# Performance work log

Measured on AMD Instinct MI355X. Metric: run time of the kernel, lower is better.

The kernel has to match this reference:

```python
import jax, jax.numpy as jnp
import numpy as np

N, H, C, E, R = 16384, 1024, 256, 16, 128
EPS = 1e-8


def setup_inputs() -> dict:
    key = jax.random.key(0)
    ks = jax.random.split(key, 8)
    s = 1.0 / np.sqrt(H)
    return {
        "x": jax.random.normal(ks[0], (N, H), jnp.float32),
        "Wd": jax.random.normal(ks[1], (H, C), jnp.float32) * s,
        "bd": jax.random.normal(ks[2], (C,), jnp.float32) * 0.01,
        "centroids": jax.random.uniform(ks[3], (E, C), jnp.float32),  # torch.rand
        "Wg": jax.random.normal(ks[4], (E, H, H), jnp.float32) * s,
        "bg": jax.random.normal(ks[5], (E, H), jnp.float32) * 0.01,
        "U": jax.random.normal(ks[6], (E, H, R), jnp.float32) * s,
        "V": jax.random.normal(ks[7], (E, R, H), jnp.float32) * (1.0 / np.sqrt(R)),
        "k": 2,
    }


def reference(x, Wd, bd, centroids, Wg, bg, U, V, k):
    # ---- Router ----
    distilled = jax.nn.gelu(x @ Wd + bd, approximate=False)          # [N, C]
    dn = distilled / jnp.maximum(
        jnp.linalg.norm(distilled, axis=-1, keepdims=True), EPS)
    cn = centroids / jnp.maximum(
        jnp.linalg.norm(centroids, axis=-1, keepdims=True), EPS)
    # cdist (euclidean) between dn [N,C] and cn [E,C]
    d2 = (jnp.sum(dn * dn, -1, keepdims=True)
          + jnp.sum(cn * cn, -1)[None, :]
          - 2.0 * (dn @ cn.T))                                        # [N, E]
    distances = jnp.sqrt(jnp.maximum(d2, 0.0))
    probabilities = jax.nn.softmax(-distances, axis=-1)               # [N, E]
    top_p, top_i = jax.lax.top_k(probabilities, k)                    # [N, k]
    # sparse combine weights: zero except at top-k experts
    combine = jnp.zeros((x.shape[0], E), x.dtype)
    combine = combine.at[jnp.arange(x.shape[0])[:, None], top_i].set(top_p)
    # ---- Expert dispatch: scan over experts (low-rank Highway blocks) ----
    def body(acc, params):
        Wg_e, bg_e, U_e, V_e, w_e = params
        gate = jax.nn.sigmoid(x @ Wg_e + bg_e)                        # [N, H]
        trans = (x @ U_e) @ V_e                                       # [N, H]
        y = gate * trans + (1.0 - gate) * x
        return acc + w_e[:, None] * y, None
    out, _ = jax.lax.scan(body, jnp.zeros_like(x),
                          (Wg, bg, U, V, combine.T))
    return out
```

## Files before the change

### kernel.cpp

```cpp
#include <hip/hip_runtime.h>
#include <hip/hip_bf16.h>
#include <cstdint>
#include <cstddef>

#define NTOK 16384
#define HD   1024
#define CD   256
#define NE   16
#define RD   128

typedef __attribute__((ext_vector_type(8))) short bf16x8;
typedef __attribute__((ext_vector_type(4))) float f32x4;
typedef unsigned short u16;
typedef unsigned int u32;

__device__ __forceinline__ u16 f2bf(float f) {
    u32 u = __float_as_uint(f);
    u32 r = (u + 0x7FFFu + ((u >> 16) & 1u)) >> 16;
    return (u16)r;
}

__device__ __forceinline__ void gload16(const void* g, void* lds) {
    __builtin_amdgcn_global_load_lds((const __attribute__((address_space(1))) void*)g,
                                     (__attribute__((address_space(3))) void*)lds,
                                     16, 0, 0);
}

__device__ __forceinline__ float wredsum(float v) {
#pragma unroll
    for (int m = 32; m >= 1; m >>= 1) v += __shfl_xor(v, m, 64);
    return v;
}

__global__ __launch_bounds__(64) void centroid_norm_kernel(
    const float* __restrict__ cen, float* __restrict__ cn, float* __restrict__ sncn)
{
    int e = blockIdx.x, l = threadIdx.x;
    float4 c = *(const float4*)&cen[e * CD + l * 4];
    float ss = wredsum(c.x * c.x + c.y * c.y + c.z * c.z + c.w * c.w);
    float den = fmaxf(sqrtf(ss), 1e-8f);
    float4 n;
    n.x = c.x / den; n.y = c.y / den; n.z = c.z / den; n.w = c.w / den;
    *(float4*)&cn[e * CD + l * 4] = n;
    float s2 = wredsum(n.x * n.x + n.y * n.y + n.z * n.z + n.w * n.w);
    if (l == 0) sncn[e] = s2;
}

__global__ __launch_bounds__(256, 4) void router_gemm_kernel(
    const float* __restrict__ x, const float* __restrict__ Wd,
    const float* __restrict__ bd, float* __restrict__ dT)
{
    __shared__ float lA[16][128];
    __shared__ float lB[16][64];
    int tid = threadIdx.x;
    int rb = (blockIdx.x >> 2) * 128;
    int cb = (blockIdx.x & 3) * 64;
    int tx = tid & 15, ty = tid >> 4;
    int arow = tid >> 1, akq = (tid & 1) * 8;
    int bk = tid >> 4, bc = (tid & 15) * 4;
    float acc[8][4];
#pragma unroll
    for (int i = 0; i < 8; ++i)
#pragma unroll
        for (int j = 0; j < 4; ++j) acc[i][j] = 0.f;

    for (int k0 = 0; k0 < HD; k0 += 16) {
        float4 a0 = *(const float4*)&x[(size_t)(rb + arow) * HD + k0 + akq];
        float4 a1 = *(const float4*)&x[(size_t)(rb + arow) * HD + k0 + akq + 4];
        float4 bv = *(const float4*)&Wd[(size_t)(k0 + bk) * CD + cb + bc];
        __syncthreads();
        lA[akq + 0][arow] = a0.x; lA[akq + 1][arow] = a0.y;
        lA[akq + 2][arow] = a0.z; lA[akq + 3][arow] = a0.w;
        lA[akq + 4][arow] = a1.x; lA[akq + 5][arow] = a1.y;
        lA[akq + 6][arow] = a1.z; lA[akq + 7][arow] = a1.w;
        *(float4*)&lB[bk][bc] = bv;
        __syncthreads();
#pragma unroll
        for (int kk = 0; kk < 16; ++kk) {
            float4 va0 = *(const float4*)&lA[kk][ty * 8];
            float4 va1 = *(const float4*)&lA[kk][ty * 8 + 4];
            float4 vb  = *(const float4*)&lB[kk][tx * 4];
            float ar[8] = {va0.x, va0.y, va0.z, va0.w, va1.x, va1.y, va1.z, va1.w};
            float br[4] = {vb.x, vb.y, vb.z, vb.w};
#pragma unroll
            for (int i = 0; i < 8; ++i)
#pragma unroll
                for (int j = 0; j < 4; ++j) acc[i][j] = fmaf(ar[i], br[j], acc[i][j]);
        }
    }
#pragma unroll
    for (int j = 0; j < 4; ++j) {
        int c = cb + tx * 4 + j;
        float b = bd[c];
        float g[8];
#pragma unroll
        for (int i = 0; i < 8; ++i) {
            float v = acc[i][j] + b;
            g[i] = 0.5f * v * (1.f + erff(v * 0.70710678118654752f));
        }
        float4 w0 = {g[0], g[1], g[2], g[3]};
        float4 w1 = {g[4], g[5], g[6], g[7]};
        *(float4*)&dT[(size_t)c * NTOK + rb + ty * 8] = w0;
        *(float4*)&dT[(size_t)c * NTOK + rb + ty * 8 + 4] = w1;
    }
}

__global__ __launch_bounds__(256) void router_score_kernel(
    const float* __restrict__ dT, const float* __restrict__ cn,
    const float* __restrict__ sncn, int* __restrict__ top_i,
    float* __restrict__ top_w, int* __restrict__ counts)
{
    __shared__ float lcn[NE][CD];
    __shared__ float sdot[NE][64];
    __shared__ float sss[64];
    __shared__ int hist[NE];
    int tid = threadIdx.x, lane = tid & 63, w = tid >> 6;
    for (int i = tid; i < NE * CD / 4; i += 256)
        ((float4*)&lcn[0][0])[i] = ((const float4*)cn)[i];
    if (tid < NE) hist[tid] = 0;
    __syncthreads();

    int tokbase = blockIdx.x * 64;
    const float* p = dT + tokbase + lane;
    int e0 = w * 4;
    float d0 = 0.f, d1 = 0.f, d2a = 0.f, d3 = 0.f, ss = 0.f;
#pragma unroll 4
    for (int k = 0; k < CD; ++k) {
        float v = p[(size_t)k * NTOK];
        ss = fmaf(v, v, ss);
        d0 = fmaf(v, lcn[e0 + 0][k], d0);
        d1 = fmaf(v, lcn[e0 + 1][k], d1);
        d2a = fmaf(v, lcn[e0 + 2][k], d2a);
        d3 = fmaf(v, lcn[e0 + 3][k], d3);
    }
    sdot[e0 + 0][lane] = d0;
    sdot[e0 + 1][lane] = d1;
    sdot[e0 + 2][lane] = d2a;
    sdot[e0 + 3][lane] = d3;
    if (w == 0) sss[lane] = ss;
    __syncthreads();

    if (tid < 64) {
        int tok = tokbase + tid;
        float ssv = sss[tid];
        float den = fmaxf(sqrtf(ssv), 1e-8f);
        float inv = 1.f / den;
        float sndn = (ssv * inv) * inv;
        float pr[NE];
#pragma unroll
        for (int e = 0; e < NE; ++e) {
            float dotn = sdot[e][tid] * inv;
            float dd2 = sndn + sncn[e] - 2.f * dotn;
            pr[e] = -sqrtf(fmaxf(dd2, 0.f));
        }
        float mx = pr[0];
#pragma unroll
        for (int e = 1; e < NE; ++e) mx = fmaxf(mx, pr[e]);
        float sum = 0.f;
#pragma unroll
        for (int e = 0; e < NE; ++e) { pr[e] = expf(pr[e] - mx); sum += pr[e]; }
        float invs = 1.f / sum;
#pragma unroll
        for (int e = 0; e < NE; ++e) pr[e] *= invs;
        int i1 = 0; float p1 = pr[0];
#pragma unroll
        for (int e = 1; e < NE; ++e) if (pr[e] > p1) { p1 = pr[e]; i1 = e; }
        int i2 = -1; float p2 = -1.f;
#pragma unroll
        for (int e = 0; e < NE; ++e) if (e != i1 && pr[e] > p2) { p2 = pr[e]; i2 = e; }
        top_i[tok * 2 + 0] = i1; top_w[tok * 2 + 0] = p1;
        top_i[tok * 2 + 1] = i2; top_w[tok * 2 + 1] = p2;
        atomicAdd(&hist[i1], 1);
        atomicAdd(&hist[i2], 1);
    }
    __syncthreads();
    if (tid < NE) atomicAdd(&counts[tid], hist[tid]);
}

__global__ void scan_kernel(const int* __restrict__ counts, int* __restrict__ offsets,
                            int* __restrict__ blkstart, int* __restrict__ cursor)
{
    if (threadIdx.x == 0 && blockIdx.x == 0) {
        int o = 0, b = 0;
        for (int e = 0; e < NE; ++e) {
            offsets[e] = o; blkstart[e] = b; cursor[e] = 0;
            o += counts[e]; b += (counts[e] + 63) >> 6;
        }
        offsets[NE] = o; blkstart[NE] = b;
    }
}

__global__ __launch_bounds__(256) void build_lists_kernel(
    const int* __restrict__ top_i, const float* __restrict__ top_w,
    const int* __restrict__ offsets, int* __restrict__ cursor,
    int* __restrict__ list_tok, float* __restrict__ list_w)
{
    int t = blockIdx.x * 256 + threadIdx.x;
#pragma unroll
    for (int j = 0; j < 2; ++j) {
        int e = top_i[t * 2 + j];
        int pos = atomicAdd(&cursor[e], 1);
        int idx = offsets[e] + pos;
        list_tok[idx] = t;
        list_w[idx] = top_w[t * 2 + j];
    }
}

__global__ __launch_bounds__(256) void cvt_bf16_kernel(
    const float* __restrict__ src, u16* __restrict__ dst, int n4)
{
    int i = blockIdx.x * 256 + threadIdx.x;
    if (i >= n4) return;
    float4 v = *(const float4*)&src[(size_t)i * 4];
    ushort4 o;
    o.x = f2bf(v.x); o.y = f2bf(v.y); o.z = f2bf(v.z); o.w = f2bf(v.w);
    *(ushort4*)&dst[(size_t)i * 4] = o;
}

__global__ __launch_bounds__(256) void transpose_cvt_kernel(
    const float* __restrict__ src, u16* __restrict__ dst, int K, int N)
{
    __shared__ float t[32][33];
    const float* s = src + (size_t)blockIdx.z * K * N;
    u16* d = dst + (size_t)blockIdx.z * K * N;
    int kb = blockIdx.y * 32, nb = blockIdx.x * 32;
    int r = threadIdx.x >> 3, c4 = (threadIdx.x & 7) * 4;
    float4 v = *(const float4*)&s[(size_t)(kb + r) * N + nb + c4];
    t[r][c4 + 0] = v.x; t[r][c4 + 1] = v.y; t[r][c4 + 2] = v.z; t[r][c4 + 3] = v.w;
    __syncthreads();
    ushort4 o;
    o.x = f2bf(t[c4 + 0][r]); o.y = f2bf(t[c4 + 1][r]);
    o.z = f2bf(t[c4 + 2][r]); o.w = f2bf(t[c4 + 3][r]);
    *(ushort4*)&d[(size_t)(nb + r) * K + kb + c4] = o;
}


__global__ __launch_bounds__(256, 3) void tproj_kernel(
    const u16* __restrict__ xbf, const u16* __restrict__ uT,
    const int* __restrict__ list_tok, const int* __restrict__ offsets,
    const int* __restrict__ blkstart, u16* __restrict__ tbf)
{
    __shared__ __align__(16) u16 lds[2 * 6144];
    __shared__ int s_tok[64];
    int mb = blockIdx.x;
    int e = 0;
#pragma unroll
    for (int i = 0; i < NE; ++i) if (mb >= blkstart[i + 1]) e = i + 1;
    if (e >= NE) return;
    int mloc = (mb - blkstart[e]) * 64;
    int base = offsets[e] + mloc;
    int cnt = offsets[e + 1] - offsets[e];
    int mv = min(64, cnt - mloc);
    int tid = threadIdx.x, lane = tid & 63, w = tid >> 6;
    if (tid < 64) s_tok[tid] = list_tok[base + (tid < mv ? tid : 0)];
    __syncthreads();
    int lrow = lane >> 2;
    int sl = (lane & 3) ^ ((lane >> 3) & 3);
    int rr = lane & 15, hi = lane >> 4;
    int rslot = hi ^ ((rr >> 1) & 3);
    const u16* uE = uT + (size_t)e * RD * HD;

    const u16* gb[3]; char* lp[3];
#pragma unroll
    for (int i = 0; i < 3; ++i) {
        int idx = w + 4 * i;
        if (idx < 4) {
            gb[i] = xbf + (size_t)s_tok[idx * 16 + lrow] * HD + sl * 8;
            lp[i] = (char*)lds + idx * 1024;
        } else {
            int bi = idx - 4;
            gb[i] = uE + (size_t)(bi * 16 + lrow) * HD + sl * 8;
            lp[i] = (char*)lds + 4096 + bi * 1024;
        }
    }
    const f32x4 zz = {0.f, 0.f, 0.f, 0.f};
    f32x4 acc[4][2];
#pragma unroll
    for (int im = 0; im < 4; ++im)
#pragma unroll
        for (int in = 0; in < 2; ++in) acc[im][in] = zz;

    auto STAGE = [&](int buf, int t) {
#pragma unroll
        for (int i = 0; i < 3; ++i) gload16(gb[i] + t * 32, lp[i] + buf * 12288);
    };
    auto COMP = [&](int buf, f32x4 (&a)[4][2]) {
        const u16* LA = lds + buf * 6144;
        const u16* LB = LA + 2048;
        bf16x8 af[4], bfv[2];
#pragma unroll
        for (int im = 0; im < 4; ++im) af[im] = *(const bf16x8*)&LA[(im * 16 + rr) * 32 + rslot * 8];
#pragma unroll
        for (int in = 0; in < 2; ++in) bfv[in] = *(const bf16x8*)&LB[(w * 32 + in * 16 + rr) * 32 + rslot * 8];
#pragma unroll
        for (int im = 0; im < 4; ++im)
#pragma unroll
            for (int in = 0; in < 2; ++in)
                a[im][in] = __builtin_amdgcn_mfma_f32_16x16x32_bf16(af[im], bfv[in], a[im][in], 0, 0, 0);
    };

    STAGE(0, 0);
    __syncthreads();
    for (int t = 0; t < 31; ++t) {
        STAGE((t + 1) & 1, t + 1);
        COMP(t & 1, acc);
        __syncthreads();
    }
    COMP(1, acc);

#pragma unroll
    for (int im = 0; im < 4; ++im)
#pragma unroll
        for (int in = 0; in < 2; ++in)
#pragma unroll
            for (int j = 0; j < 4; ++j) {
                int r = im * 16 + hi * 4 + j;
                if (r < mv) {
                    int c = w * 32 + in * 16 + rr;
                    tbf[(size_t)(base + r) * RD + c] = f2bf(acc[im][in][j]);
                }
            }
}

__global__ __launch_bounds__(256, 3) void expert_kernel(
    const u16* __restrict__ xbf, const u16* __restrict__ wgT,
    const u16* __restrict__ vT, const u16* __restrict__ tbf,
    const float* __restrict__ x, const float* __restrict__ bg,
    const int* __restrict__ list_tok, const float* __restrict__ list_w,
    const int* __restrict__ offsets, const int* __restrict__ blkstart,
    float* __restrict__ out)
{
    __shared__ __align__(16) u16 lds[2 * 6144];
    __shared__ int s_tok[64];
    __shared__ float s_w[64];
    int mb = blockIdx.x >> 3, ct = blockIdx.x & 7;
    int e = 0;
#pragma unroll
    for (int i = 0; i < NE; ++i) if (mb >= blkstart[i + 1]) e = i + 1;
    if (e >= NE) return;
    int mloc = (mb - blkstart[e]) * 64;
    int base = offsets[e] + mloc;
    int cnt = offsets[e + 1] - offsets[e];
    int mv = min(64, cnt - mloc);
    int tid = threadIdx.x, lane = tid & 63, w = tid >> 6;
    if (tid < 64) {
        int p = base + (tid < mv ? tid : 0);
        s_tok[tid] = list_tok[p];
        s_w[tid] = (tid < mv) ? list_w[p] : 0.f;
    }
    __syncthreads();
    int lrow = lane >> 2;
    int sl = (lane & 3) ^ ((lane >> 3) & 3);
    int rr = lane & 15, hi = lane >> 4;
    int rslot = hi ^ ((rr >> 1) & 3);

    const u16* wgE = wgT + (size_t)e * HD * HD + (size_t)(ct * 128) * HD;
    const u16* vE  = vT  + (size_t)e * HD * RD + (size_t)(ct * 128) * RD;

    char* lp[3];
    const u16* gbT[3]; const u16* gbG[3];
#pragma unroll
    for (int i = 0; i < 3; ++i) {
        int idx = w + 4 * i;
        if (idx < 4) {
            lp[i]  = (char*)lds + idx * 1024;
            gbT[i] = tbf + (size_t)(base + idx * 16 + lrow) * RD + sl * 8;
            gbG[i] = xbf + (size_t)s_tok[idx * 16 + lrow] * HD + sl * 8;
        } else {
            int bi = idx - 4;
            lp[i]  = (char*)lds + 4096 + bi * 1024;
            gbT[i] = vE  + (size_t)(bi * 16 + lrow) * RD + sl * 8;
            gbG[i] = wgE + (size_t)(bi * 16 + lrow) * HD + sl * 8;
        }
    }

    auto STAGE = [&](int buf, int t, const u16* const (&gb)[3]) {
#pragma unroll
        for (int i = 0; i < 3; ++i) gload16(gb[i] + t * 32, lp[i] + buf * 12288);
    };
    auto COMP = [&](int buf, f32x4 (&a)[4][2]) {
        const u16* LA = lds + buf * 6144;
        const u16* LB = LA + 2048;
        bf16x8 af[4], bfv[2];
#pragma unroll
        for (int im = 0; im < 4; ++im) af[im] = *(const bf16x8*)&LA[(im * 16 + rr) * 32 + rslot * 8];
#pragma unroll
        for (int in = 0; in < 2; ++in) bfv[in] = *(const bf16x8*)&LB[(w * 32 + in * 16 + rr) * 32 + rslot * 8];
#pragma unroll
        for (int im = 0; im < 4; ++im)
#pragma unroll
            for (int in = 0; in < 2; ++in)
                a[im][in] = __builtin_amdgcn_mfma_f32_16x16x32_bf16(af[im], bfv[in], a[im][in], 0, 0, 0);
    };

    const f32x4 zz = {0.f, 0.f, 0.f, 0.f};
    f32x4 accT[4][2];
#pragma unroll
    for (int im = 0; im < 4; ++im)
#pragma unroll
        for (int in = 0; in < 2; ++in) accT[im][in] = zz;

    STAGE(0, 0, gbT);
    __syncthreads();
#pragma unroll
    for (int t = 0; t < 3; ++t) {
        STAGE((t + 1) & 1, t + 1, gbT);
        COMP(t & 1, accT);
        __syncthreads();
    }
    STAGE(0, 0, gbG);
    COMP(1, accT);
    __syncthreads();

    f32x4 accG[4][2];
#pragma unroll
    for (int im = 0; im < 4; ++im)
#pragma unroll
        for (int in = 0; in < 2; ++in) accG[im][in] = zz;

    for (int t = 0; t < 31; ++t) {
        STAGE((t + 1) & 1, t + 1, gbG);
        COMP(t & 1, accG);
        __syncthreads();
    }
    COMP(1, accG);

    float bgv[2];
#pragma unroll
    for (int in = 0; in < 2; ++in)
        bgv[in] = bg[e * HD + ct * 128 + w * 32 + in * 16 + rr];

#pragma unroll
    for (int im = 0; im < 4; ++im)
#pragma unroll
        for (int j = 0; j < 4; ++j) {
            int r = im * 16 + hi * 4 + j;
            if (r < mv) {
                int tok = s_tok[r];
                float wgt = s_w[r];
                size_t rowoff = (size_t)tok * HD;
#pragma unroll
                for (int in = 0; in < 2; ++in) {
                    int c = ct * 128 + w * 32 + in * 16 + rr;
                    float gp = accG[im][in][j] + bgv[in];
                    float sg = 1.f / (1.f + __expf(-gp));
                    float tr = accT[im][in][j];
                    float xv = x[rowoff + c];
                    float yv = sg * tr + (1.f - sg) * xv;
                    atomicAdd(&out[rowoff + c], wgt * yv);
                }
            }
        }
}

extern "C" void kernel_launch(void* const* d_in, const int* in_sizes, int n_in,
                              void* d_out, int out_size, void* d_ws, size_t ws_size,
                              hipStream_t stream)
{
    const float* x   = (const float*)d_in[0];
    const float* Wd  = (const float*)d_in[1];
    const float* bd  = (const float*)d_in[2];
    const float* cen = (const float*)d_in[3];
    const float* Wg  = (const float*)d_in[4];
    const float* bg  = (const float*)d_in[5];
    const float* U   = (const float*)d_in[6];
    const float* V   = (const float*)d_in[7];
    float* out = (float*)d_out;

    char* ws = (char*)d_ws;
    size_t off = 0;
    auto alloc = [&](size_t bytes) { size_t o = off; off = (off + bytes + 255) & ~(size_t)255; return o; };
    float* dT        = (float*)(ws + alloc((size_t)NTOK * CD * 4));
    float* cn        = (float*)(ws + alloc((size_t)NE * CD * 4));
    float* sncn      = (float*)(ws + alloc(NE * 4));
    int*   top_i     = (int*)(ws + alloc((size_t)NTOK * 2 * 4));
    float* top_w     = (float*)(ws + alloc((size_t)NTOK * 2 * 4));
    int*   counts    = (int*)(ws + alloc(NE * 4));
    int*   offsets   = (int*)(ws + alloc((NE + 1) * 4));
    int*   blkstart  = (int*)(ws + alloc((NE + 1) * 4));
    int*   cursor    = (int*)(ws + alloc(NE * 4));
    int*   list_tok  = (int*)(ws + alloc((size_t)NTOK * 2 * 4));
    float* list_w    = (float*)(ws + alloc((size_t)NTOK * 2 * 4));
    u16*   xbf       = (u16*)(ws + alloc((size_t)NTOK * HD * 2));
    u16*   wgT       = (u16*)(ws + alloc((size_t)NE * HD * HD * 2));
    u16*   uT        = (u16*)(ws + alloc((size_t)NE * RD * HD * 2));
    u16*   vT        = (u16*)(ws + alloc((size_t)NE * RD * HD * 2));
    u16*   tbf       = (u16*)(ws + alloc(((size_t)NTOK * 2 + 64) * RD * 2));

    hipMemsetAsync(out, 0, (size_t)out_size * 4, stream);
    hipMemsetAsync(counts, 0, NE * 4, stream);

    centroid_norm_kernel<<<NE, 64, 0, stream>>>(cen, cn, sncn);
    router_gemm_kernel<<<(NTOK / 128) * 4, 256, 0, stream>>>(x, Wd, bd, dT);
    router_score_kernel<<<NTOK / 64, 256, 0, stream>>>(dT, cn, sncn, top_i, top_w, counts);
    scan_kernel<<<1, 64, 0, stream>>>(counts, offsets, blkstart, cursor);
    build_lists_kernel<<<NTOK / 256, 256, 0, stream>>>(top_i, top_w, offsets, cursor, list_tok, list_w);

    cvt_bf16_kernel<<<(NTOK * HD / 4 + 255) / 256, 256, 0, stream>>>(x, xbf, NTOK * HD / 4);
    transpose_cvt_kernel<<<dim3(HD / 32, HD / 32, NE), 256, 0, stream>>>(Wg, wgT, HD, HD);
    transpose_cvt_kernel<<<dim3(RD / 32, HD / 32, NE), 256, 0, stream>>>(U, uT, HD, RD);
    transpose_cvt_kernel<<<dim3(HD / 32, RD / 32, NE), 256, 0, stream>>>(V, vT, RD, HD);

    int maxblk = NTOK * 2 / 64 + NE;
    tproj_kernel<<<maxblk, 256, 0, stream>>>(xbf, uT, list_tok, offsets, blkstart, tbf);
    expert_kernel<<<maxblk * 8, 256, 0, stream>>>(xbf, wgT, vT, tbf, x, bg,
                                                  list_tok, list_w, offsets, blkstart, out);
}
```

Measured before the change: 579.1 us.

## Widen expert tile to 256 columns, remap blocks for XCD locality, reorder gate/trans GEMMs

The expert kernel's per-block output width doubles from 128 to 256 columns (4x4 MFMA accumulators per wave), so each staged token tile is reused across twice as many weight columns and x-row gathers are halved. Block indices are remapped so blocks sharing a column tile are grouped, presumably for L2/XCD locality. The gate GEMM now runs first, with its sigmoid results packed to fp16 to free registers before the trans accumulation. The costs are higher register pressure, more LDS per block, lower occupancy, and fp16 rounding of the gate values.

```diff
diff --git a/kernel.cpp b/kernel.cpp
--- a/kernel.cpp
+++ b/kernel.cpp
@@ -1,5 +1,6 @@
 #include <hip/hip_runtime.h>
 #include <hip/hip_bf16.h>
+#include <hip/hip_fp16.h>
 #include <cstdint>
 #include <cstddef>
 
@@ -8,6 +9,8 @@
 #define CD   256
 #define NE   16
 #define RD   128
+#define MAXBLK 528
+#define EGRID  2304
 
 typedef __attribute__((ext_vector_type(8))) short bf16x8;
 typedef __attribute__((ext_vector_type(4))) float f32x4;
@@ -330,10 +333,14 @@
     const int* __restrict__ offsets, const int* __restrict__ blkstart,
     float* __restrict__ out)
 {
-    __shared__ __align__(16) u16 lds[2 * 6144];
+    __shared__ __align__(16) u16 lds[2 * 10240];
     __shared__ int s_tok[64];
     __shared__ float s_w[64];
-    int mb = blockIdx.x >> 3, ct = blockIdx.x & 7;
+    int d = blockIdx.x;
+    int l = (d >> 8) * 256 + (d & 7) * 32 + ((d & 255) >> 3);
+    if (l >= 4 * MAXBLK) return;
+    int ct = l / MAXBLK;
+    int mb = l % MAXBLK;
     int e = 0;
 #pragma unroll
     for (int i = 0; i < NE; ++i) if (mb >= blkstart[i + 1]) e = i + 1;
@@ -354,13 +361,13 @@
     int rr = lane & 15, hi = lane >> 4;
     int rslot = hi ^ ((rr >> 1) & 3);
 
-    const u16* wgE = wgT + (size_t)e * HD * HD + (size_t)(ct * 128) * HD;
-    const u16* vE  = vT  + (size_t)e * HD * RD + (size_t)(ct * 128) * RD;
-
-    char* lp[3];
-    const u16* gbT[3]; const u16* gbG[3];
-#pragma unroll
-    for (int i = 0; i < 3; ++i) {
+    const u16* wgE = wgT + (size_t)e * HD * HD + (size_t)(ct * 256) * HD;
+    const u16* vE  = vT  + (size_t)e * HD * RD + (size_t)(ct * 256) * RD;
+
+    char* lp[5];
+    const u16* gbT[5]; const u16* gbG[5];
+#pragma unroll
+    for (int i = 0; i < 5; ++i) {
         int idx = w + 4 * i;
         if (idx < 4) {
             lp[i]  = (char*)lds + idx * 1024;
@@ -374,61 +381,71 @@
         }
     }
 
-    auto STAGE = [&](int buf, int t, const u16* const (&gb)[3]) {
-#pragma unroll
-        for (int i = 0; i < 3; ++i) gload16(gb[i] + t * 32, lp[i] + buf * 12288);
+    auto STAGE = [&](int buf, int t, const u16* const (&gb)[5]) {
+#pragma unroll
+        for (int i = 0; i < 5; ++i) gload16(gb[i] + t * 32, lp[i] + buf * 20480);
     };
-    auto COMP = [&](int buf, f32x4 (&a)[4][2]) {
-        const u16* LA = lds + buf * 6144;
+    auto COMP = [&](int buf, f32x4 (&a)[4][4]) {
+        const u16* LA = lds + buf * 10240;
         const u16* LB = LA + 2048;
-        bf16x8 af[4], bfv[2];
+        bf16x8 af[4], bfv[4];
 #pragma unroll
         for (int im = 0; im < 4; ++im) af[im] = *(const bf16x8*)&LA[(im * 16 + rr) * 32 + rslot * 8];
 #pragma unroll
-        for (int in = 0; in < 2; ++in) bfv[in] = *(const bf16x8*)&LB[(w * 32 + in * 16 + rr) * 32 + rslot * 8];
+        for (int in = 0; in < 4; ++in) bfv[in] = *(const bf16x8*)&LB[(w * 64 + in * 16 + rr) * 32 + rslot * 8];
 #pragma unroll
         for (int im = 0; im < 4; ++im)
 #pragma unroll
-            for (int in = 0; in < 2; ++in)
+            for (int in = 0; in < 4; ++in)
                 a[im][in] = __builtin_amdgcn_mfma_f32_16x16x32_bf16(af[im], bfv[in], a[im][in], 0, 0, 0);
     };
 
     const f32x4 zz = {0.f, 0.f, 0.f, 0.f};
-    f32x4 accT[4][2];
+    float bgv[4];
+#pragma unroll
+    for (int in = 0; in < 4; ++in)
+        bgv[in] = bg[e * HD + ct * 256 + w * 64 + in * 16 + rr];
+
+    f32x4 accG[4][4];
 #pragma unroll
     for (int im = 0; im < 4; ++im)
 #pragma unroll
-        for (int in = 0; in < 2; ++in) accT[im][in] = zz;
-
-    STAGE(0, 0, gbT);
-    __syncthreads();
-#pragma unroll
-    for (int t = 0; t < 3; ++t) {
-        STAGE((t + 1) & 1, t + 1, gbT);
-        COMP(t & 1, accT);
-        __syncthreads();
-    }
+        for (int in = 0; in < 4; ++in) accG[im][in] = zz;
+
     STAGE(0, 0, gbG);
-    COMP(1, accT);
-    __syncthreads();
-
-    f32x4 accG[4][2];
-#pragma unroll
-    for (int im = 0; im < 4; ++im)
-#pragma unroll
-        for (int in = 0; in < 2; ++in) accG[im][in] = zz;
-
-    for (int t = 0; t < 31; ++t) {
-        STAGE((t + 1) & 1, t + 1, gbG);
+    __syncthreads();
+    for (int t = 0; t < 32; ++t) {
+        if (t < 31) STAGE((t + 1) & 1, t + 1, gbG);
+        else        STAGE(0, 0, gbT);
         COMP(t & 1, accG);
         __syncthreads();
     }
-    COMP(1, accG);
-
-    float bgv[2];
-#pragma unroll
-    for (int in = 0; in < 2; ++in)
-        bgv[in] = bg[e * HD + ct * 128 + w * 32 + in * 16 + rr];
+
+    __half2 sgp[4][4][2];
+#pragma unroll
+    for (int im = 0; im < 4; ++im)
+#pragma unroll
+        for (int in = 0; in < 4; ++in) {
+            float s0 = 1.f / (1.f + __expf(-(accG[im][in][0] + bgv[in])));
+            float s1 = 1.f / (1.f + __expf(-(accG[im][in][1] + bgv[in])));
+            float s2 = 1.f / (1.f + __expf(-(accG[im][in][2] + bgv[in])));
+            float s3 = 1.f / (1.f + __expf(-(accG[im][in][3] + bgv[in])));
+            sgp[im][in][0] = __floats2half2_rn(s0, s1);
+            sgp[im][in][1] = __floats2half2_rn(s2, s3);
+        }
+
+    f32x4 accT[4][4];
+#pragma unroll
+    for (int im = 0; im < 4; ++im)
+#pragma unroll
+        for (int in = 0; in < 4; ++in) accT[im][in] = zz;
+
+#pragma unroll
+    for (int s = 0; s < 4; ++s) {
+        if (s < 3) STAGE((s + 1) & 1, s + 1, gbT);
+        COMP(s & 1, accT);
+        __syncthreads();
+    }
 
 #pragma unroll
     for (int im = 0; im < 4; ++im)
@@ -440,10 +457,10 @@
                 float wgt = s_w[r];
                 size_t rowoff = (size_t)tok * HD;
 #pragma unroll
-                for (int in = 0; in < 2; ++in) {
-                    int c = ct * 128 + w * 32 + in * 16 + rr;
-                    float gp = accG[im][in][j] + bgv[in];
-                    float sg = 1.f / (1.f + __expf(-gp));
+                for (int in = 0; in < 4; ++in) {
+                    int c = ct * 256 + w * 64 + in * 16 + rr;
+                    float2 sq = __half22float2(sgp[im][in][j >> 1]);
+                    float sg = (j & 1) ? sq.y : sq.x;
                     float tr = accT[im][in][j];
                     float xv = x[rowoff + c];
                     float yv = sg * tr + (1.f - sg) * xv;
@@ -501,8 +518,7 @@
     transpose_cvt_kernel<<<dim3(RD / 32, HD / 32, NE), 256, 0, stream>>>(U, uT, HD, RD);
     transpose_cvt_kernel<<<dim3(HD / 32, RD / 32, NE), 256, 0, stream>>>(V, vT, RD, HD);
 
-    int maxblk = NTOK * 2 / 64 + NE;
-    tproj_kernel<<<maxblk, 256, 0, stream>>>(xbf, uT, list_tok, offsets, blkstart, tbf);
-    expert_kernel<<<maxblk * 8, 256, 0, stream>>>(xbf, wgT, vT, tbf, x, bg,
-                                                  list_tok, list_w, offsets, blkstart, out);
-}
+    tproj_kernel<<<MAXBLK, 256, 0, stream>>>(xbf, uT, list_tok, offsets, blkstart, tbf);
+    expert_kernel<<<EGRID, 256, 0, stream>>>(xbf, wgT, vT, tbf, x, bg,
+                                             list_tok, list_w, offsets, blkstart, out);
+}
```

New measurement: 601.8 us. 3.9% more time.
